# Kernel optimization log

Measured on AMD Instinct MI355X. Metric: run time of the kernel, lower is better.

The kernel has to match this reference:

```python
import jax, jax.numpy as jnp
import numpy as np

E = 512  # encoding_dim
B = 2048
T = 100
FUTURE = 10
POSE = 34


def _lstm_cell(x, h, c, Wih, Whh, bih, bhh):
    # torch LSTMCell: gates = x @ Wih^T + bih + h @ Whh^T + bhh, order i,f,g,o
    gates = x @ Wih.T + h @ Whh.T + (bih + bhh)  # [B, 4E]
    i, f, g, o = jnp.split(gates, 4, axis=-1)
    i = jax.nn.sigmoid(i)
    f = jax.nn.sigmoid(f)
    g = jnp.tanh(g)
    o = jax.nn.sigmoid(o)
    c_new = f * c + i * g
    h_new = o * jnp.tanh(c_new)
    return h_new, c_new


def setup_inputs() -> dict:
    key = jax.random.key(0)
    ks = jax.random.split(key, 20)
    s = 1.0 / np.sqrt(E)
    d = {
        "x": jax.random.normal(ks[0], (B, T, POSE), dtype=jnp.float32),
        "enc_lin_W": jax.random.uniform(ks[1], (E, POSE), jnp.float32, -s, s),
        "enc_lin_b": jax.random.uniform(ks[2], (E,), jnp.float32, -s, s),
        "enc1_Wih": jax.random.uniform(ks[3], (4 * E, E), jnp.float32, -s, s),
        "enc1_Whh": jax.random.uniform(ks[4], (4 * E, E), jnp.float32, -s, s),
        "enc1_bih": jax.random.uniform(ks[5], (4 * E,), jnp.float32, -s, s),
        "enc1_bhh": jax.random.uniform(ks[6], (4 * E,), jnp.float32, -s, s),
        "enc2_Wih": jax.random.uniform(ks[7], (4 * E, E), jnp.float32, -s, s),
        "enc2_Whh": jax.random.uniform(ks[8], (4 * E, E), jnp.float32, -s, s),
        "enc2_bih": jax.random.uniform(ks[9], (4 * E,), jnp.float32, -s, s),
        "enc2_bhh": jax.random.uniform(ks[10], (4 * E,), jnp.float32, -s, s),
        "dec1_Wih": jax.random.uniform(ks[11], (4 * E, E), jnp.float32, -s, s),
        "dec1_Whh": jax.random.uniform(ks[12], (4 * E, E), jnp.float32, -s, s),
        "dec1_bih": jax.random.uniform(ks[13], (4 * E,), jnp.float32, -s, s),
        "dec1_bhh": jax.random.uniform(ks[14], (4 * E,), jnp.float32, -s, s),
        "dec_lin_W": jax.random.uniform(ks[15], (POSE, E), jnp.float32, -s, s),
        "dec_lin_b": jax.random.uniform(ks[16], (POSE,), jnp.float32, -s, s),
    }
    return d


def reference(x, enc_lin_W, enc_lin_b,
              enc1_Wih, enc1_Whh, enc1_bih, enc1_bhh,
              enc2_Wih, enc2_Whh, enc2_bih, enc2_bhh,
              dec1_Wih, dec1_Whh, dec1_bih, dec1_bhh,
              dec_lin_W, dec_lin_b):
    bsz = x.shape[0]
    # ---- encoder ----
    enc = x @ enc_lin_W.T + enc_lin_b                  # [B, T, E]
    enc_t = jnp.swapaxes(enc, 0, 1)                    # [T, B, E]
    z = jnp.zeros((bsz, E), dtype=x.dtype)

    def enc_step(carry, xt):
        h1, c1, h2, c2 = carry
        h1, c1 = _lstm_cell(xt, h1, c1, enc1_Wih, enc1_Whh, enc1_bih, enc1_bhh)
        h2, c2 = _lstm_cell(h1, h2, c2, enc2_Wih, enc2_Whh, enc2_bih, enc2_bhh)
        return (h1, c1, h2, c2), None

    (h1, c1, h2, c2), _ = jax.lax.scan(enc_step, (z, z, z, z), enc_t)

    # ---- decoder (zeros start token; lstm2 of decoder is unused in forward) ----
    def dec_step(carry, _):
        h, c, out = carry
        h, c = _lstm_cell(out, h, c, dec1_Wih, dec1_Whh, dec1_bih, dec1_bhh)
        return (h, c, h), h

    _, hs = jax.lax.scan(dec_step, (h2, c2, z), None, length=FUTURE)  # [F, B, E]
    preds = jnp.swapaxes(hs, 0, 1)                     # [B, F, E]
    return preds @ dec_lin_W.T + dec_lin_b             # [B, F, 34]
```

## Files before the change

kernel.cpp:

```cpp
#include <hip/hip_runtime.h>


#define TSEQ 100
#define FUT 10
#define POSE_D 34
#define EDIM 512
#define BDIM 2048

typedef __bf16 bf16x8 __attribute__((ext_vector_type(8)));
typedef float floatx4 __attribute__((ext_vector_type(4)));
typedef short shortx8 __attribute__((ext_vector_type(8)));

__device__ __forceinline__ float bf2f(short s) {
    unsigned int u = ((unsigned int)(unsigned short)s) << 16;
    float f;
    __builtin_memcpy(&f, &u, 4);
    return f;
}
__device__ __forceinline__ short f2bf(float f) {
    unsigned int u;
    __builtin_memcpy(&u, &f, 4);
    u += 0x7fffu + ((u >> 16) & 1u);
    return (short)(u >> 16);
}
__device__ __forceinline__ float fsig(float x) { return 1.f / (1.f + __expf(-x)); }
__device__ __forceinline__ float ftanh(float x) {
    float ax = fabsf(x);
    float t = __expf(-2.f * ax);
    float r = (1.f - t) / (1.f + t);
    return x < 0.f ? -r : r;
}


__global__ __launch_bounds__(512, 2) void fused_step_kernel(
    const float* __restrict__ xnext, const short* __restrict__ M1,
    const short* __restrict__ h1, const short* __restrict__ sWhh1,
    const short* __restrict__ sWih2, const short* __restrict__ h2,
    const short* __restrict__ sWhh2,
    const float* __restrict__ bias1, const float* __restrict__ bias2,
    float* __restrict__ c1, float* __restrict__ c2,
    short* __restrict__ h1_out, short* __restrict__ h2_out) {
    __shared__ __align__(16) short lds[73728];
    const int tid = threadIdx.x;
    const int lane = tid & 63;
    const int wv = tid >> 6;
    const int es2 = wv & 1;
    const int rb = (wv >> 1) & 1;
    const int cs = wv >> 2;
    const int m = lane & 15;
    const int q = lane >> 4;
    const int e16 = blockIdx.x & 15;
    const int R0 = (blockIdx.x >> 4) * 128;
    const int e0 = e16 >> 1;
    const int es = (e16 & 1) * 2 + es2;
    constexpr int AOFF = 8192;

    floatx4 acc[4][4];
#pragma unroll
    for (int ri = 0; ri < 4; ++ri)
#pragma unroll
        for (int g = 0; g < 4; ++g) acc[ri][g] = {0.f, 0.f, 0.f, 0.f};

    bf16x8 rW0[8], rW1[8];

    auto loadW = [&](const short* __restrict__ W, int kcp, bf16x8(&w_)[8]) {
        const short* P = W + (long)((e0 * 16 + kcp) * 4 + es) * 4096 + lane * 8;
#pragma unroll
        for (int i = 0; i < 8; ++i) w_[i] = *(const bf16x8*)(P + i * 512);
    };
    auto do_chunk = [&](int kcp, bf16x8(&w_)[8]) {
        const int k8 = (kcp & 7) * 8;
#pragma unroll
        for (int kk = 0; kk < 2; ++kk) {
            bf16x8 a[4];
#pragma unroll
            for (int ri = 0; ri < 4; ++ri) {
                const int row = rb * 64 + ri * 16 + m;
                a[ri] = *(const bf16x8*)(lds + AOFF + row * 512 +
                                         ((k8 | (((kk * 4 + q) ^ row) & 7)) << 3));
            }
#pragma unroll
            for (int ri = 0; ri < 4; ++ri)
#pragma unroll
                for (int g = 0; g < 4; ++g)
                    acc[ri][g] = __builtin_amdgcn_mfma_f32_16x16x32_bf16(
                        a[ri], w_[g * 2 + kk], acc[ri][g], 0, 0, 0);
        }
    };
    auto do_x = [&](bf16x8(&w_)[8]) {
#pragma unroll
        for (int kk = 0; kk < 2; ++kk) {
            bf16x8 a[4];
#pragma unroll
            for (int ri = 0; ri < 4; ++ri) {
                const int row = rb * 64 + ri * 16 + m;
                a[ri] = *(const bf16x8*)(lds + row * 64 + (((kk * 4 + q) ^ (row & 7)) << 3));
            }
#pragma unroll
            for (int ri = 0; ri < 4; ++ri)
#pragma unroll
                for (int g = 0; g < 4; ++g)
                    acc[ri][g] = __builtin_amdgcn_mfma_f32_16x16x32_bf16(
                        a[ri], w_[g * 2 + kk], acc[ri][g], 0, 0, 0);
        }
    };
    auto stageA = [&](const short* __restrict__ G) {
#pragma unroll
        for (int i = 0; i < 16; ++i) {
            const int u = tid + (i << 9);
            const int r = u >> 6, c = u & 63;
            const shortx8 v = *(const shortx8*)(G + (long)r * 512 + (c << 3));
            *(shortx8*)(lds + AOFF + r * 512 + (((c & 56) | ((c ^ r) & 7)) << 3)) = v;
        }
    };
    auto epilogue = [&](const float* __restrict__ bias, float* __restrict__ c_io,
                        short* __restrict__ h_out) {
        const int e = e16 * 32 + es2 * 16 + m;
        const float bi = bias[e];
        const float bfv = bias[512 + e];
        const float bg = bias[1024 + e];
        const float bo = bias[1536 + e];
#pragma unroll
        for (int ri = 0; ri < 4; ++ri) {
#pragma unroll
            for (int rg = 0; rg < 4; ++rg) {
                const int br = R0 + rb * 64 + ri * 16 + q * 4 + rg;
                const long cidx = (long)br * EDIM + e;
                const float iv = fsig(acc[ri][0][rg] + bi);
                const float fv = fsig(acc[ri][1][rg] + bfv);
                const float gv = ftanh(acc[ri][2][rg] + bg);
                const float ov = fsig(acc[ri][3][rg] + bo);
                const float cn = fv * c_io[cidx] + iv * gv;
                c_io[cidx] = cn;
                h_out[cidx] = f2bf(ov * ftanh(cn));
            }
        }
    };

    floatx4 z = {0.f, 0.f, 0.f, 0.f};
    *(floatx4*)(lds + tid * 16) = z;
    *(floatx4*)(lds + tid * 16 + 8) = z;
    stageA(h1 + (long)R0 * 512);
    __syncthreads();
    for (int idx = tid; idx < 128 * POSE_D; idx += 512) {
        const int r = idx / POSE_D;
        const int c = idx - r * POSE_D;
        lds[r * 64 + (((c >> 3) ^ (r & 7)) << 3) + (c & 7)] =
            f2bf(xnext[(long)(R0 + r) * (TSEQ * POSE_D) + c]);
    }
    if (cs == 0) {
        const short* P = M1 + (long)((e0 * 4 + es) * 8) * 512 + lane * 8;
#pragma unroll
        for (int i = 0; i < 8; ++i) rW0[i] = *(const bf16x8*)(P + i * 512);
        loadW(sWhh1, 0, rW1);
    } else {
        loadW(sWih2, 0, rW0);
        loadW(sWih2, 1, rW1);
    }
    __syncthreads();

    if (cs == 0) {
        do_x(rW0);
#pragma unroll 1
        for (int k = 0; k < 8; ++k) {
            bf16x8(&buf)[8] = (k & 1) ? rW0 : rW1;
            do_chunk(k, buf);
            if (k + 2 < 8) loadW(sWhh1, k + 2, buf);
        }
    } else {
#pragma unroll 1
        for (int k = 0; k < 8; ++k) {
            bf16x8(&buf)[8] = (k & 1) ? rW1 : rW0;
            do_chunk(k, buf);
            if (k + 2 < 8) loadW(sWih2, k + 2, buf);
        }
    }

    __syncthreads();
    stageA(h2 + (long)R0 * 512);
    if (cs == 1) {
        loadW(sWhh2, 0, rW0);
        loadW(sWhh2, 1, rW1);
    }
    __syncthreads();

    if (cs == 0) {
        epilogue(bias1, c1, h1_out);
    } else {
#pragma unroll 1
        for (int k = 0; k < 8; ++k) {
            bf16x8(&buf)[8] = (k & 1) ? rW1 : rW0;
            do_chunk(k, buf);
            if (k + 2 < 8) loadW(sWhh2, k + 2, buf);
        }
        epilogue(bias2, c2, h2_out);
    }
}

template <bool HAS_X, bool TWO_H, int NP>
__global__ __launch_bounds__(512, 2) void lstm_cell_kernel(
    const float* __restrict__ xptr, const short* __restrict__ M1,
    const short* __restrict__ A1, const short* __restrict__ W1,
    const short* __restrict__ A2, const short* __restrict__ W2,
    const float* __restrict__ bias, float* __restrict__ c_io,
    short* __restrict__ h_out, float* __restrict__ hf_out) {
    __shared__ __align__(16) short lds[HAS_X ? 73728 : 65536];
    const int tid = threadIdx.x;
    const int lane = tid & 63;
    const int wv = tid >> 6;
    const int es2 = wv & 1;
    const int rb = (wv >> 1) & 1;
    const int kg = wv >> 2;
    const int m = lane & 15;
    const int q = lane >> 4;
    const int e16 = blockIdx.x & 15;
    const int R0 = (blockIdx.x >> 4) * 128;
    const int e0 = e16 >> 1;
    const int es = (e16 & 1) * 2 + es2;
    constexpr int PH = NP * 8;
    constexpr int AOFF = HAS_X ? 8192 : 0;

    floatx4 acc[4][4];
#pragma unroll
    for (int ri = 0; ri < 4; ++ri)
#pragma unroll
        for (int g = 0; g < 4; ++g) acc[ri][g] = {0.f, 0.f, 0.f, 0.f};

    bf16x8 rW0[8], rW1[8];

    auto loadW = [&](const short* __restrict__ W, int kcp, bf16x8(&w_)[8]) {
        const short* P = W + (long)((e0 * 16 + kcp) * 4 + es) * 4096 + lane * 8;
#pragma unroll
        for (int i = 0; i < 8; ++i) w_[i] = *(const bf16x8*)(P + i * 512);
    };
    auto loadM1 = [&](bf16x8(&w_)[8]) {
        const short* P = M1 + (long)((e0 * 4 + es) * 8) * 512 + lane * 8;
#pragma unroll
        for (int i = 0; i < 8; ++i) w_[i] = *(const bf16x8*)(P + i * 512);
    };
    auto do_chunk = [&](int kcp, bf16x8(&w_)[8]) {
        const int k8 = (kcp & 7) * 8;
#pragma unroll
        for (int kk = 0; kk < 2; ++kk) {
            bf16x8 a[4];
#pragma unroll
            for (int ri = 0; ri < 4; ++ri) {
                const int row = rb * 64 + ri * 16 + m;
                a[ri] = *(const bf16x8*)(lds + AOFF + row * 512 +
                                         ((k8 | (((kk * 4 + q) ^ row) & 7)) << 3));
            }
#pragma unroll
            for (int ri = 0; ri < 4; ++ri)
#pragma unroll
                for (int g = 0; g < 4; ++g)
                    acc[ri][g] = __builtin_amdgcn_mfma_f32_16x16x32_bf16(
                        a[ri], w_[g * 2 + kk], acc[ri][g], 0, 0, 0);
        }
    };
    auto do_x = [&](bf16x8(&w_)[8]) {
#pragma unroll
        for (int kk = 0; kk < 2; ++kk) {
            bf16x8 a[4];
#pragma unroll
            for (int ri = 0; ri < 4; ++ri) {
                const int row = rb * 64 + ri * 16 + m;
                a[ri] = *(const bf16x8*)(lds + row * 64 + (((kk * 4 + q) ^ (row & 7)) << 3));
            }
#pragma unroll
            for (int ri = 0; ri < 4; ++ri)
#pragma unroll
                for (int g = 0; g < 4; ++g)
                    acc[ri][g] = __builtin_amdgcn_mfma_f32_16x16x32_bf16(
                        a[ri], w_[g * 2 + kk], acc[ri][g], 0, 0, 0);
        }
    };
    auto stageA = [&](const short* __restrict__ G, int dst) {
#pragma unroll
        for (int i = 0; i < 16; ++i) {
            const int u = tid + (i << 9);
            const int r = u >> 6, c = u & 63;
            const shortx8 v = *(const shortx8*)(G + (long)r * 512 + (c << 3));
            *(shortx8*)(lds + dst + r * 512 + (((c & 56) | ((c ^ r) & 7)) << 3)) = v;
        }
    };
    auto loopP = [&](const short* __restrict__ W) {
        int c = kg;
#pragma unroll 1
        for (;;) {
            const int nxt = c + 2;
            if (nxt < PH) loadW(W, nxt, rW1);
            do_chunk(c, rW0);
            c = nxt;
            if (c >= PH) break;
            const int nx2 = c + 2;
            if (nx2 < PH) loadW(W, nx2, rW0);
            do_chunk(c, rW1);
            c = nx2;
            if (c >= PH) break;
        }
    };

    if constexpr (HAS_X) {
        constexpr int NT = 1 + PH;
        floatx4 z = {0.f, 0.f, 0.f, 0.f};
        *(floatx4*)(lds + tid * 16) = z;
        *(floatx4*)(lds + tid * 16 + 8) = z;
        stageA(A1 + (long)R0 * 512, AOFF);
        __syncthreads();
        for (int idx = tid; idx < 128 * POSE_D; idx += 512) {
            const int r = idx / POSE_D;
            const int c = idx - r * POSE_D;
            lds[r * 64 + (((c >> 3) ^ (r & 7)) << 3) + (c & 7)] =
                f2bf(xptr[(long)(R0 + r) * (TSEQ * POSE_D) + c]);
        }
        if (kg == 0) loadM1(rW0);
        else loadW(W1, 0, rW0);
        __syncthreads();
        int c = kg;
#pragma unroll 1
        for (;;) {
            const int nxt = c + 2;
            if (nxt < NT) loadW(W1, nxt - 1, rW1);
            if (c == 0) do_x(rW0);
            else do_chunk(c - 1, rW0);
            c = nxt;
            if (c >= NT) break;
            const int nx2 = c + 2;
            if (nx2 < NT) loadW(W1, nx2 - 1, rW0);
            do_chunk(c - 1, rW1);
            c = nx2;
            if (c >= NT) break;
        }
    } else {
        stageA(A1 + (long)R0 * 512, AOFF);
        loadW(W1, kg, rW0);
        __syncthreads();
        loopP(W1);
        if constexpr (TWO_H) {
            __syncthreads();
            stageA(A2 + (long)R0 * 512, AOFF);
            loadW(W2, kg, rW0);
            __syncthreads();
            loopP(W2);
        }
    }

    __syncthreads();
    float* ldsf = (float*)lds;
    const int L = (rb * 2 + es2) * 64 + lane;
    if (kg == 1) {
#pragma unroll
        for (int ri = 0; ri < 4; ++ri)
#pragma unroll
            for (int g = 0; g < 4; ++g) {
                const int f4 = ri * 4 + g;
                *(floatx4*)(ldsf + L * 68 + ((f4 ^ m) << 2)) = acc[ri][g];
            }
    }
    __syncthreads();
    if (kg == 0) {
#pragma unroll
        for (int ri = 0; ri < 4; ++ri)
#pragma unroll
            for (int g = 0; g < 4; ++g) {
                const int f4 = ri * 4 + g;
                acc[ri][g] += *(const floatx4*)(ldsf + L * 68 + ((f4 ^ m) << 2));
            }
        const int e = e16 * 32 + es2 * 16 + m;
        const float bi = bias[e];
        const float bfv = bias[512 + e];
        const float bg = bias[1024 + e];
        const float bo = bias[1536 + e];
#pragma unroll
        for (int ri = 0; ri < 4; ++ri) {
#pragma unroll
            for (int rg = 0; rg < 4; ++rg) {
                const int br = R0 + rb * 64 + ri * 16 + q * 4 + rg;
                const long cidx = (long)br * EDIM + e;
                const float iv = fsig(acc[ri][0][rg] + bi);
                const float fv = fsig(acc[ri][1][rg] + bfv);
                const float gv = ftanh(acc[ri][2][rg] + bg);
                const float ov = fsig(acc[ri][3][rg] + bo);
                const float cn = fv * c_io[cidx] + iv * gv;
                c_io[cidx] = cn;
                const float hv = ov * ftanh(cn);
                h_out[cidx] = f2bf(hv);
                if (hf_out) hf_out[cidx] = hv;
            }
        }
    }
}

__global__ __launch_bounds__(256) void zero_kernel(unsigned int* __restrict__ p, int n) {
    int i = blockIdx.x * 256 + threadIdx.x;
    const int stride = gridDim.x * 256;
    for (; i < n; i += stride) p[i] = 0u;
}

__global__ __launch_bounds__(256) void prep_bias(
    const float* __restrict__ bih1, const float* __restrict__ bhh1,
    const float* __restrict__ Wih1, const float* __restrict__ encb,
    const float* __restrict__ bih2, const float* __restrict__ bhh2,
    const float* __restrict__ dbih, const float* __restrict__ dbhh,
    float* __restrict__ bias1, float* __restrict__ bias2, float* __restrict__ biasd) {
    const int n = blockIdx.x * 256 + threadIdx.x;
    if (n >= 2048) return;
    float s = bih1[n] + bhh1[n];
    const float* wr = Wih1 + (long)n * EDIM;
    for (int j = 0; j < EDIM; ++j) s += wr[j] * encb[j];
    bias1[n] = s;
    bias2[n] = bih2[n] + bhh2[n];
    biasd[n] = dbih[n] + dbhh[n];
}

__global__ __launch_bounds__(256) void swizzle_w(const float* __restrict__ a,
                                                 const float* __restrict__ b,
                                                 short* __restrict__ o, int nkc) {
    const int idx = blockIdx.x * 256 + threadIdx.x;
    if (idx >= 262144) return;
    const int lane = idx & 63, kk = (idx >> 6) & 1, g = (idx >> 7) & 3;
    const int w = (idx >> 9) & 3, kc = (idx >> 11) & 15, e0 = idx >> 15;
    if (kc >= nkc) return;
    const int row = g * 512 + e0 * 64 + w * 16 + (lane & 15);
    const int ks = (kc & 7) * 64 + kk * 32 + (lane >> 4) * 8;
    const bool lo = kc >= 8;
    shortx8 outv;
#pragma unroll
    for (int j = 0; j < 8; ++j) {
        const long si = (long)row * EDIM + ks + j;
        const float v = b ? (a[si] + b[si]) : a[si];
        const short hi = f2bf(v);
        outv[j] = lo ? f2bf(v - bf2f(hi)) : hi;
    }
    *(shortx8*)(o + (long)idx * 8) = outv;
}

__global__ __launch_bounds__(256) void swizzle_M1(const float* __restrict__ Wih1,
                                                  const float* __restrict__ encW,
                                                  short* __restrict__ o) {
    const int idx = blockIdx.x * 256 + threadIdx.x;
    if (idx >= 131072) return;
    const int u = idx >> 3, j = idx & 7;
    const int lane = u & 63, kk = (u >> 6) & 1, g = (u >> 7) & 3;
    const int w = (u >> 9) & 3, e0 = u >> 11;
    const int row = g * 512 + e0 * 64 + w * 16 + (lane & 15);
    const int k = kk * 32 + (lane >> 4) * 8 + j;
    float s = 0.f;
    if (k < POSE_D) {
        const float* wr = Wih1 + (long)row * EDIM;
        for (int jj = 0; jj < EDIM; ++jj) s += wr[jj] * encW[jj * POSE_D + k];
    }
    o[(long)u * 8 + j] = f2bf(s);
}

__global__ __launch_bounds__(64) void out_proj(const float* __restrict__ hf,
                                               const float* __restrict__ W,
                                               const float* __restrict__ bias,
                                               float* __restrict__ out, int f) {
    const int b = blockIdx.x;
    __shared__ float hrow[EDIM];
    const int lane = threadIdx.x;
    *(floatx4*)(hrow + lane * 8) = *(const floatx4*)(hf + (long)b * EDIM + lane * 8);
    *(floatx4*)(hrow + lane * 8 + 4) = *(const floatx4*)(hf + (long)b * EDIM + lane * 8 + 4);
    __syncthreads();
    if (lane < POSE_D) {
        float acc = bias[lane];
        const float* wr = W + (long)lane * EDIM;
        for (int e = 0; e < EDIM; e += 4) {
            const floatx4 wv = *(const floatx4*)(wr + e);
            acc += hrow[e] * wv[0] + hrow[e + 1] * wv[1] + hrow[e + 2] * wv[2] + hrow[e + 3] * wv[3];
        }
        out[((long)b * FUT + f) * POSE_D + lane] = acc;
    }
}

extern "C" void kernel_launch(void* const* d_in, const int* in_sizes, int n_in,
                              void* d_out, int out_size, void* d_ws, size_t ws_size,
                              hipStream_t stream) {
    const float* x = (const float*)d_in[0];
    const float* encW = (const float*)d_in[1];
    const float* encb = (const float*)d_in[2];
    const float* Wih1 = (const float*)d_in[3];
    const float* Whh1 = (const float*)d_in[4];
    const float* bih1 = (const float*)d_in[5];
    const float* bhh1 = (const float*)d_in[6];
    const float* Wih2 = (const float*)d_in[7];
    const float* Whh2 = (const float*)d_in[8];
    const float* bih2 = (const float*)d_in[9];
    const float* bhh2 = (const float*)d_in[10];
    const float* dWih = (const float*)d_in[11];
    const float* dWhh = (const float*)d_in[12];
    const float* dbih = (const float*)d_in[13];
    const float* dbhh = (const float*)d_in[14];
    const float* oW = (const float*)d_in[15];
    const float* ob = (const float*)d_in[16];
    float* out = (float*)d_out;

    char* ws = (char*)d_ws;
    size_t off = 0;
    auto alloc = [&](size_t bytes) -> char* {
        char* p = ws + off;
        off = (off + bytes + 255) & ~(size_t)255;
        return p;
    };
    const size_t HB = (size_t)BDIM * EDIM * 2;
    const size_t CB = (size_t)BDIM * EDIM * 4;
    const size_t WSZ = (size_t)262144 * 16;
    short* h1_0 = (short*)alloc(HB);
    short* h2_0 = (short*)alloc(HB);
    float* c1 = (float*)alloc(CB);
    float* c2 = (float*)alloc(CB);
    short* h1_1 = (short*)alloc(HB);
    short* h2_1 = (short*)alloc(HB);
    float* hf0 = (float*)alloc(CB);
    float* hf1 = (float*)alloc(CB);
    short* M1 = (short*)alloc((size_t)16384 * 16);
    short* sWhh1 = (short*)alloc(WSZ);
    short* sWih2 = (short*)alloc(WSZ);
    short* sWhh2 = (short*)alloc(WSZ);
    short* sdWhh = (short*)alloc(WSZ);
    short* sWsum = (short*)alloc(WSZ);
    float* bias1 = (float*)alloc(2048 * 4);
    float* bias2 = (float*)alloc(2048 * 4);
    float* biasd = (float*)alloc(2048 * 4);
    (void)ws_size; (void)in_sizes; (void)n_in; (void)out_size;

    zero_kernel<<<2048, 256, 0, stream>>>((unsigned int*)h1_0, (int)((2 * HB + 2 * CB) / 4));
    prep_bias<<<8, 256, 0, stream>>>(bih1, bhh1, Wih1, encb, bih2, bhh2, dbih, dbhh,
                                     bias1, bias2, biasd);
    swizzle_M1<<<512, 256, 0, stream>>>(Wih1, encW, M1);
    swizzle_w<<<1024, 256, 0, stream>>>(Whh1, nullptr, sWhh1, 8);
    swizzle_w<<<1024, 256, 0, stream>>>(Wih2, nullptr, sWih2, 8);
    swizzle_w<<<1024, 256, 0, stream>>>(Whh2, nullptr, sWhh2, 8);
    swizzle_w<<<1024, 256, 0, stream>>>(dWhh, nullptr, sdWhh, 16);
    swizzle_w<<<1024, 256, 0, stream>>>(dWih, dWhh, sWsum, 16);

    dim3 grid(256), blk(512);
    lstm_cell_kernel<true, false, 1><<<grid, blk, 0, stream>>>(
        x, M1, h1_0, sWhh1, nullptr, nullptr, bias1, c1, h1_1, nullptr);
    short *h1c = h1_1, *h1n = h1_0, *h2c = h2_0, *h2n = h2_1;
    for (int t = 0; t < TSEQ - 1; ++t) {
        fused_step_kernel<<<grid, blk, 0, stream>>>(
            x + (t + 1) * POSE_D, M1, h1c, sWhh1, sWih2, h2c, sWhh2,
            bias1, bias2, c1, c2, h1n, h2n);
        short* s1 = h1c; h1c = h1n; h1n = s1;
        short* s2 = h2c; h2c = h2n; h2n = s2;
    }
    lstm_cell_kernel<false, true, 1><<<grid, blk, 0, stream>>>(
        nullptr, nullptr, h1c, sWih2, h2c, sWhh2, bias2, c2, h2n, nullptr);
    short* h2fin = h2n;

    short* hd0 = h1c;
    short* hd1 = h1n;
    lstm_cell_kernel<false, false, 2><<<grid, blk, 0, stream>>>(
        nullptr, nullptr, h2fin, sdWhh, nullptr, nullptr, biasd, c2, hd0, hf0);
    out_proj<<<BDIM, 64, 0, stream>>>(hf0, oW, ob, out, 0);
    short *dp = hd0, *dn = hd1;
    float *fp = hf0, *fn = hf1;
    for (int f = 1; f < FUT; ++f) {
        lstm_cell_kernel<false, false, 2><<<grid, blk, 0, stream>>>(
            nullptr, nullptr, dp, sWsum, nullptr, nullptr, biasd, c2, dn, fn);
        out_proj<<<BDIM, 64, 0, stream>>>(fn, oW, ob, out, f);
        short* tt = dp; dp = dn; dn = tt;
        float* tf = fp; fp = fn; fn = tf;
    }
}
```

Before: 3.480 ms.

## Fuse encoder timesteps into persistent cooperative kernel with grid barrier

```diff
diff --git a/kernel.cpp b/kernel.cpp
--- a/kernel.cpp
+++ b/kernel.cpp
@@ -32,14 +32,13 @@
 }
 
 
-__global__ __launch_bounds__(512, 2) void fused_step_kernel(
-    const float* __restrict__ xnext, const short* __restrict__ M1,
-    const short* __restrict__ h1, const short* __restrict__ sWhh1,
-    const short* __restrict__ sWih2, const short* __restrict__ h2,
-    const short* __restrict__ sWhh2,
-    const float* __restrict__ bias1, const float* __restrict__ bias2,
-    float* __restrict__ c1, float* __restrict__ c2,
-    short* __restrict__ h1_out, short* __restrict__ h2_out) {
+__global__ __launch_bounds__(512, 2) void seq_persistent(
+    const float* __restrict__ x, const short* __restrict__ M1,
+    const short* __restrict__ sWhh1, const short* __restrict__ sWih2,
+    const short* __restrict__ sWhh2, const float* __restrict__ bias1,
+    const float* __restrict__ bias2, short* __restrict__ h1a,
+    short* __restrict__ h1b, short* __restrict__ h2a, short* __restrict__ h2b,
+    float* __restrict__ c2out, unsigned int* __restrict__ cnt) {
     __shared__ __align__(16) short lds[73728];
     const int tid = threadIdx.x;
     const int lane = tid & 63;
@@ -55,12 +54,11 @@
     const int es = (e16 & 1) * 2 + es2;
     constexpr int AOFF = 8192;
 
+    float creg[16];
+#pragma unroll
+    for (int i = 0; i < 16; ++i) creg[i] = 0.f;
+
     floatx4 acc[4][4];
-#pragma unroll
-    for (int ri = 0; ri < 4; ++ri)
-#pragma unroll
-        for (int g = 0; g < 4; ++g) acc[ri][g] = {0.f, 0.f, 0.f, 0.f};
-
     bf16x8 rW0[8], rW1[8];
 
     auto loadW = [&](const short* __restrict__ W, int kcp, bf16x8(&w_)[8]) {
@@ -109,12 +107,20 @@
         for (int i = 0; i < 16; ++i) {
             const int u = tid + (i << 9);
             const int r = u >> 6, c = u & 63;
-            const shortx8 v = *(const shortx8*)(G + (long)r * 512 + (c << 3));
-            *(shortx8*)(lds + AOFF + r * 512 + (((c & 56) | ((c ^ r) & 7)) << 3)) = v;
-        }
-    };
-    auto epilogue = [&](const float* __restrict__ bias, float* __restrict__ c_io,
-                        short* __restrict__ h_out) {
+            const unsigned long long* s =
+                (const unsigned long long*)(G + (long)r * 512 + (c << 3));
+            unsigned long long v0 =
+                __hip_atomic_load(s, __ATOMIC_RELAXED, __HIP_MEMORY_SCOPE_AGENT);
+            unsigned long long v1 =
+                __hip_atomic_load(s + 1, __ATOMIC_RELAXED, __HIP_MEMORY_SCOPE_AGENT);
+            unsigned long long* d = (unsigned long long*)(
+                lds + AOFF + r * 512 + (((c & 56) | ((c ^ r) & 7)) << 3));
+            d[0] = v0;
+            d[1] = v1;
+        }
+    };
+    auto epilogue = [&](const float* __restrict__ bias, short* __restrict__ h_out,
+                        float* __restrict__ c_out) {
         const int e = e16 * 32 + es2 * 16 + m;
         const float bi = bias[e];
         const float bfv = bias[512 + e];
@@ -130,70 +136,120 @@
                 const float fv = fsig(acc[ri][1][rg] + bfv);
                 const float gv = ftanh(acc[ri][2][rg] + bg);
                 const float ov = fsig(acc[ri][3][rg] + bo);
-                const float cn = fv * c_io[cidx] + iv * gv;
-                c_io[cidx] = cn;
-                h_out[cidx] = f2bf(ov * ftanh(cn));
-            }
-        }
-    };
-
-    floatx4 z = {0.f, 0.f, 0.f, 0.f};
-    *(floatx4*)(lds + tid * 16) = z;
-    *(floatx4*)(lds + tid * 16 + 8) = z;
-    stageA(h1 + (long)R0 * 512);
+                float& cc = creg[ri * 4 + rg];
+                const float cn = fv * cc + iv * gv;
+                cc = cn;
+                const int hvi = (int)f2bf(ov * ftanh(cn));
+                asm volatile("global_store_short %0, %1, off sc0 sc1" ::"v"(h_out + cidx),
+                             "v"(hvi)
+                             : "memory");
+                if (c_out) c_out[cidx] = cn;
+            }
+        }
+    };
+
+    {
+        floatx4 z = {0.f, 0.f, 0.f, 0.f};
+        *(floatx4*)(lds + tid * 16) = z;
+        *(floatx4*)(lds + tid * 16 + 8) = z;
+    }
     __syncthreads();
-    for (int idx = tid; idx < 128 * POSE_D; idx += 512) {
-        const int r = idx / POSE_D;
-        const int c = idx - r * POSE_D;
-        lds[r * 64 + (((c >> 3) ^ (r & 7)) << 3) + (c & 7)] =
-            f2bf(xnext[(long)(R0 + r) * (TSEQ * POSE_D) + c]);
-    }
-    if (cs == 0) {
-        const short* P = M1 + (long)((e0 * 4 + es) * 8) * 512 + lane * 8;
-#pragma unroll
-        for (int i = 0; i < 8; ++i) rW0[i] = *(const bf16x8*)(P + i * 512);
-        loadW(sWhh1, 0, rW1);
-    } else {
-        loadW(sWih2, 0, rW0);
-        loadW(sWih2, 1, rW1);
-    }
-    __syncthreads();
-
-    if (cs == 0) {
-        do_x(rW0);
+
+    short* const h1buf[2] = {h1a, h1b};
+    short* const h2buf[2] = {h2a, h2b};
+
 #pragma unroll 1
-        for (int k = 0; k < 8; ++k) {
-            bf16x8(&buf)[8] = (k & 1) ? rW0 : rW1;
-            do_chunk(k, buf);
-            if (k + 2 < 8) loadW(sWhh1, k + 2, buf);
-        }
-    } else {
+    for (int it = 0; it <= TSEQ; ++it) {
+        const bool do1 = (it < TSEQ);
+        const bool doh = (it >= 1);
+        const short* rd1 = h1buf[(it & 1) ^ 1];
+        const short* rd2 = h2buf[it & 1];
+        short* wr1 = h1buf[it & 1];
+        short* wr2 = h2buf[(it & 1) ^ 1];
+
+        if (doh) stageA(rd1 + (long)R0 * 512);
+        if (do1) {
+            const float* xit = x + (long)it * POSE_D;
+            for (int idx = tid; idx < 128 * POSE_D; idx += 512) {
+                const int r = idx / POSE_D;
+                const int c = idx - r * POSE_D;
+                lds[r * 64 + (((c >> 3) ^ (r & 7)) << 3) + (c & 7)] =
+                    f2bf(xit[(long)(R0 + r) * (TSEQ * POSE_D) + c]);
+            }
+        }
+        if (cs == 0) {
+            if (do1) {
+                const short* P = M1 + (long)((e0 * 4 + es) * 8) * 512 + lane * 8;
+#pragma unroll
+                for (int i = 0; i < 8; ++i) rW0[i] = *(const bf16x8*)(P + i * 512);
+                if (doh) loadW(sWhh1, 0, rW1);
+            }
+        } else if (doh) {
+            loadW(sWih2, 0, rW0);
+            loadW(sWih2, 1, rW1);
+        }
+#pragma unroll
+        for (int ri = 0; ri < 4; ++ri)
+#pragma unroll
+            for (int g = 0; g < 4; ++g) acc[ri][g] = {0.f, 0.f, 0.f, 0.f};
+        __syncthreads();
+
+        if (cs == 0) {
+            if (do1) {
+                do_x(rW0);
+                if (doh) {
 #pragma unroll 1
-        for (int k = 0; k < 8; ++k) {
-            bf16x8(&buf)[8] = (k & 1) ? rW1 : rW0;
-            do_chunk(k, buf);
-            if (k + 2 < 8) loadW(sWih2, k + 2, buf);
-        }
-    }
-
-    __syncthreads();
-    stageA(h2 + (long)R0 * 512);
-    if (cs == 1) {
-        loadW(sWhh2, 0, rW0);
-        loadW(sWhh2, 1, rW1);
-    }
-    __syncthreads();
-
-    if (cs == 0) {
-        epilogue(bias1, c1, h1_out);
-    } else {
+                    for (int k = 0; k < 8; ++k) {
+                        bf16x8(&buf)[8] = (k & 1) ? rW0 : rW1;
+                        do_chunk(k, buf);
+                        if (k + 2 < 8) loadW(sWhh1, k + 2, buf);
+                    }
+                }
+            }
+        } else if (doh) {
 #pragma unroll 1
-        for (int k = 0; k < 8; ++k) {
-            bf16x8(&buf)[8] = (k & 1) ? rW1 : rW0;
-            do_chunk(k, buf);
-            if (k + 2 < 8) loadW(sWhh2, k + 2, buf);
-        }
-        epilogue(bias2, c2, h2_out);
+            for (int k = 0; k < 8; ++k) {
+                bf16x8(&buf)[8] = (k & 1) ? rW1 : rW0;
+                do_chunk(k, buf);
+                if (k + 2 < 8) loadW(sWih2, k + 2, buf);
+            }
+        }
+
+        __syncthreads();
+        if (doh) {
+            stageA(rd2 + (long)R0 * 512);
+            if (cs == 1) {
+                loadW(sWhh2, 0, rW0);
+                loadW(sWhh2, 1, rW1);
+            }
+        }
+        __syncthreads();
+
+        if (cs == 0) {
+            if (do1) epilogue(bias1, wr1, nullptr);
+        } else if (doh) {
+#pragma unroll 1
+            for (int k = 0; k < 8; ++k) {
+                bf16x8(&buf)[8] = (k & 1) ? rW1 : rW0;
+                do_chunk(k, buf);
+                if (k + 2 < 8) loadW(sWhh2, k + 2, buf);
+            }
+            epilogue(bias2, wr2, (it == TSEQ) ? c2out : nullptr);
+        }
+
+        if (it < TSEQ) {
+            asm volatile("s_waitcnt vmcnt(0)" ::: "memory");
+            __syncthreads();
+            if (tid == 0) {
+                __hip_atomic_fetch_add(cnt, 1u, __ATOMIC_RELAXED,
+                                       __HIP_MEMORY_SCOPE_AGENT);
+                const unsigned tgt = 256u * (unsigned)(it + 1);
+                while (__hip_atomic_load(cnt, __ATOMIC_RELAXED,
+                                         __HIP_MEMORY_SCOPE_AGENT) < tgt)
+                    __builtin_amdgcn_s_sleep(2);
+            }
+            __syncthreads();
+        }
     }
 }
 
@@ -506,12 +562,12 @@
     const size_t HB = (size_t)BDIM * EDIM * 2;
     const size_t CB = (size_t)BDIM * EDIM * 4;
     const size_t WSZ = (size_t)262144 * 16;
-    short* h1_0 = (short*)alloc(HB);
-    short* h2_0 = (short*)alloc(HB);
-    float* c1 = (float*)alloc(CB);
+    short* h2b = (short*)alloc(HB);
+    unsigned int* cnt = (unsigned int*)alloc(256);
+    short* h1a = (short*)alloc(HB);
+    short* h1b = (short*)alloc(HB);
+    short* h2a = (short*)alloc(HB);
     float* c2 = (float*)alloc(CB);
-    short* h1_1 = (short*)alloc(HB);
-    short* h2_1 = (short*)alloc(HB);
     float* hf0 = (float*)alloc(CB);
     float* hf1 = (float*)alloc(CB);
     short* M1 = (short*)alloc((size_t)16384 * 16);
@@ -525,7 +581,7 @@
     float* biasd = (float*)alloc(2048 * 4);
     (void)ws_size; (void)in_sizes; (void)n_in; (void)out_size;
 
-    zero_kernel<<<2048, 256, 0, stream>>>((unsigned int*)h1_0, (int)((2 * HB + 2 * CB) / 4));
+    zero_kernel<<<2048, 256, 0, stream>>>((unsigned int*)h2b, (int)((HB + 256) / 4));
     prep_bias<<<8, 256, 0, stream>>>(bih1, bhh1, Wih1, encb, bih2, bhh2, dbih, dbhh,
                                      bias1, bias2, biasd);
     swizzle_M1<<<512, 256, 0, stream>>>(Wih1, encW, M1);
@@ -535,25 +591,21 @@
     swizzle_w<<<1024, 256, 0, stream>>>(dWhh, nullptr, sdWhh, 16);
     swizzle_w<<<1024, 256, 0, stream>>>(dWih, dWhh, sWsum, 16);
 
+    {
+        void* kargs[] = {&x,     &M1,    &sWhh1, &sWih2, &sWhh2, &bias1, &bias2,
+                         &h1a,   &h1b,   &h2a,   &h2b,   &c2,    &cnt};
+        if (hipLaunchCooperativeKernel((void*)seq_persistent, dim3(256), dim3(512),
+                                       kargs, 0, stream) != hipSuccess) {
+            seq_persistent<<<dim3(256), dim3(512), 0, stream>>>(
+                x, M1, sWhh1, sWih2, sWhh2, bias1, bias2, h1a, h1b, h2a, h2b, c2, cnt);
+        }
+    }
+
     dim3 grid(256), blk(512);
-    lstm_cell_kernel<true, false, 1><<<grid, blk, 0, stream>>>(
-        x, M1, h1_0, sWhh1, nullptr, nullptr, bias1, c1, h1_1, nullptr);
-    short *h1c = h1_1, *h1n = h1_0, *h2c = h2_0, *h2n = h2_1;
-    for (int t = 0; t < TSEQ - 1; ++t) {
-        fused_step_kernel<<<grid, blk, 0, stream>>>(
-            x + (t + 1) * POSE_D, M1, h1c, sWhh1, sWih2, h2c, sWhh2,
-            bias1, bias2, c1, c2, h1n, h2n);
-        short* s1 = h1c; h1c = h1n; h1n = s1;
-        short* s2 = h2c; h2c = h2n; h2n = s2;
-    }
-    lstm_cell_kernel<false, true, 1><<<grid, blk, 0, stream>>>(
-        nullptr, nullptr, h1c, sWih2, h2c, sWhh2, bias2, c2, h2n, nullptr);
-    short* h2fin = h2n;
-
-    short* hd0 = h1c;
-    short* hd1 = h1n;
+    short* hd0 = h1a;
+    short* hd1 = h1b;
     lstm_cell_kernel<false, false, 2><<<grid, blk, 0, stream>>>(
-        nullptr, nullptr, h2fin, sdWhh, nullptr, nullptr, biasd, c2, hd0, hf0);
+        nullptr, nullptr, h2b, sdWhh, nullptr, nullptr, biasd, c2, hd0, hf0);
     out_proj<<<BDIM, 64, 0, stream>>>(hf0, oW, ob, out, 0);
     short *dp = hd0, *dn = hd1;
     float *fp = hf0, *fn = hf1;
```

New measurement: 5.531 ms. +58.9%, slower.
